# Performance work log

Hardware: AMD Instinct MI355X
Metric: run time of the kernel (lower is better)

Reference implementation:

```python
import jax, jax.numpy as jnp
import numpy as np

EPS = 1e-8


def l2norm(x, axis):
    # matches torch: x / (sqrt(sum(x^2)) + eps)
    return x / (jnp.sqrt(jnp.sum(x * x, axis=axis, keepdims=True)) + EPS)


def setup_inputs() -> dict:
    key = jax.random.key(0)
    k1, k2, k3, k4, k5 = jax.random.split(key, 5)
    I, C, L, R, D = 16, 32, 32, 36, 1024  # n_image, n_caption, max_words, n_regions, embed_dim
    img_emb = l2norm(jax.random.normal(k1, (I, R, D), jnp.float32), -1)
    cap_emb = l2norm(jax.random.normal(k2, (C, L, D), jnp.float32), -1)
    W_emb = jax.random.normal(k3, (D, D), jnp.float32)  # nn.Embedding weight, N(0,1) default init
    sim_map_w = 2.5 + 0.1 * jax.random.normal(k4, (1, D), jnp.float32)  # init_weight: normal(2.5, 0.1)
    temp_scale_w = jnp.full((1, 1), np.log(1.0 / 0.07), jnp.float32)    # init_weight
    temp_learnable_w = jnp.full((1, 1), 4.0, jnp.float32)               # init_weight
    cap_lens = jax.random.randint(k5, (C,), 4, L + 1, jnp.int32)        # ragged caption lengths in [4, L]
    return dict(img_emb=img_emb, cap_emb=cap_emb, W_emb=W_emb, sim_map_w=sim_map_w,
                temp_scale_w=temp_scale_w, temp_learnable_w=temp_learnable_w, cap_lens=cap_lens)


def reference(img_emb, cap_emb, W_emb, sim_map_w, temp_scale_w, temp_learnable_w, cap_lens):
    D = W_emb.shape[0]
    L = cap_emb.shape[1]
    # --- dimension-weight branch (caption-independent) ---
    # linspace(0, D, D).long(): last index is D (out of range in torch); gather with clip.
    idx = jnp.floor(jnp.linspace(0.0, D, D)).astype(jnp.int32)
    weights = jax.nn.sigmoid(jnp.take(W_emb, idx, axis=0, mode='clip'))  # (D, D)
    mean_p = jnp.mean(weights, axis=1)                  # (D,)
    std_p = jnp.std(weights, axis=1, ddof=1)            # torch.std is unbiased
    thres = mean_p + sim_map_w[0] * std_p               # (D,)
    values = jnp.exp(temp_learnable_w[0, 0]) * (weights - thres[:, None])
    mask_p = jnp.tanh(jnp.exp(values))
    Dlw = l2norm(mask_p * weights, axis=1)              # Dim_learned_weights (D, D)
    diag = Dlw.sum(0)                                   # Diagonal (D,); diag_embed matmul == elementwise scale
    smooth = jnp.exp(temp_scale_w[0, 0])
    # --- vectorized ragged per-caption cross attention ---
    wmask = (jnp.arange(L)[None, :] < cap_lens[:, None]).astype(cap_emb.dtype)  # (C, L)
    # attn[c,i,l,r] = tanh(sum_d cap[c,l,d] * diag[d] * img[i,r,d])
    attn = jnp.tanh(jnp.einsum('cld,ird->cilr', cap_emb, img_emb * diag))
    attn = jnp.where(attn >= 0, attn, 0.1 * attn) * wmask[:, None, :, None]  # LeakyReLU(0.1), zero padded words
    attn = attn / (jnp.sqrt(jnp.sum(attn * attn, axis=2, keepdims=True)) + EPS)  # l2norm over word dim
    attn = jax.nn.softmax(attn * smooth, axis=3)        # softmax over regions
    ctx = l2norm(jnp.einsum('cilr,ird->cild', attn, img_emb), axis=-1)  # Context_img
    sim_loc = ctx * cap_emb[:, None, :, :]
    sim_sub = jnp.einsum('cild,ed->cile', sim_loc, Dlw)  # sim_loc @ Dlw.T
    sim_vec = l2norm(sim_sub, axis=-1).sum(-1)           # (C, I, L)
    # mean over the n_word valid words of each caption
    sim = jnp.sum(sim_vec * wmask[:, None, :], axis=2) / cap_lens[:, None].astype(cap_emb.dtype)  # (C, I)
    return sim.T  # (n_image, n_caption), matching torch.cat(sim_all, 1)
```

## Files before the change

kernel.cpp:

```cpp
#include <hip/hip_runtime.h>
#include <hip/hip_bf16.h>

#define I_N 16
#define C_N 32
#define L_N 32
#define R_N 36
#define D_N 1024
#define EPSF 1e-8f

typedef _Float16 f16;
typedef __attribute__((ext_vector_type(8))) _Float16 half8;
typedef __attribute__((ext_vector_type(4))) float floatx4;

__device__ __forceinline__ void gl16(const f16* g, f16* l) {
  __builtin_amdgcn_global_load_lds(
      (const __attribute__((address_space(1))) void*)g,
      (__attribute__((address_space(3))) void*)l, 16, 0, 0);
}

__device__ __forceinline__ float fast_tanh(float x) {
  float q = __expf(-2.f * fabsf(x));
  float t = (1.f - q) / (1.f + q);
  return (x >= 0.f) ? t : -t;
}

__device__ __forceinline__ float blk_sum_256(float v, float* red) {
  #pragma unroll
  for (int off = 32; off > 0; off >>= 1) v += __shfl_down(v, off, 64);
  int wid = threadIdx.x >> 6;
  if ((threadIdx.x & 63) == 0) red[wid] = v;
  __syncthreads();
  float s = red[0] + red[1] + red[2] + red[3];
  __syncthreads();
  return s;
}

__global__ __launch_bounds__(256) void k_dlw(const float* __restrict__ W,
    const float* __restrict__ simw, const float* __restrict__ tlw,
    float* __restrict__ Dlw, f16* __restrict__ DlwH) {
  int row = blockIdx.x, tid = threadIdx.x;
  __shared__ float red[4];
  const float* Wr = W + (size_t)row * D_N;
  float w[4]; float p = 0.f;
  #pragma unroll
  for (int k = 0; k < 4; ++k) {
    int j = tid + k * 256;
    float x = Wr[j];
    w[k] = 1.f / (1.f + __expf(-x));
    p += w[k];
  }
  float S = blk_sum_256(p, red);
  float mean = S * (1.f / 1024.f);
  p = 0.f;
  #pragma unroll
  for (int k = 0; k < 4; ++k) { float d = w[k] - mean; p += d * d; }
  float S2 = blk_sum_256(p, red);
  float stdv = sqrtf(S2 * (1.f / 1023.f));
  float thres = mean + simw[row] * stdv;
  float eT = __expf(tlw[0]);
  float mw[4]; p = 0.f;
  #pragma unroll
  for (int k = 0; k < 4; ++k) {
    float val = eT * (w[k] - thres);
    float y = __expf(val);
    float q = __expf(-2.f * y);
    float mp = (1.f - q) / (1.f + q);
    mw[k] = mp * w[k];
    p += mw[k] * mw[k];
  }
  float S3 = blk_sum_256(p, red);
  float inv = 1.f / (sqrtf(S3) + EPSF);
  #pragma unroll
  for (int k = 0; k < 4; ++k) {
    int j = tid + k * 256;
    float v = mw[k] * inv;
    Dlw[(size_t)row * D_N + j] = v;
    DlwH[(size_t)row * D_N + j] = (f16)v;
  }
}

__global__ __launch_bounds__(256) void k_diag_part(const float* __restrict__ Dlw,
                                                   float* __restrict__ dpart) {
  int col = blockIdx.x * 256 + threadIdx.x;
  int p = blockIdx.y;
  float s = 0.f;
  #pragma unroll 8
  for (int r = p * 64; r < p * 64 + 64; ++r) s += Dlw[(size_t)r * D_N + col];
  dpart[(size_t)p * D_N + col] = s;
}

__global__ __launch_bounds__(256) void k_diag2p(const float* __restrict__ dpart,
    const int* __restrict__ lens, float* __restrict__ diag,
    int* __restrict__ pfx, int* __restrict__ mp) {
  if (blockIdx.x < 4) {
    int col = blockIdx.x * 256 + threadIdx.x;
    float s = 0.f;
    #pragma unroll
    for (int p = 0; p < 16; ++p) s += dpart[(size_t)p * D_N + col];
    diag[col] = s;
  } else if (threadIdx.x < 64) {
    int l = threadIdx.x;
    int v = (l < 32) ? lens[l] : 0;
    int s = v;
    #pragma unroll
    for (int off = 1; off < 32; off <<= 1) {
      int t = __shfl_up(s, off, 64);
      if (l >= off) s += t;
    }
    if (l < 32) pfx[l] = s - v;
    if (l == 31) { pfx[32] = s; mp[0] = s * 16; }
  }
}

__global__ __launch_bounds__(256) void k_prep(const float* __restrict__ cap,
    const float* __restrict__ img, const float* __restrict__ diag,
    f16* __restrict__ capH, f16* __restrict__ imgH, f16* __restrict__ imgdH) {
  int bid = blockIdx.x;
  if (bid < 1024) {
    size_t base = (size_t)bid * D_N;
    #pragma unroll
    for (int k = 0; k < 4; ++k) {
      int j = threadIdx.x + k * 256;
      capH[base + j] = (f16)cap[base + j];
    }
  } else if (bid < 1600) {
    size_t base = (size_t)(bid - 1024) * D_N;
    #pragma unroll
    for (int k = 0; k < 4; ++k) {
      int j = threadIdx.x + k * 256;
      imgH[base + j] = (f16)img[base + j];
    }
  } else {
    int row = bid - 1600;
    int i = row / 48, r = row % 48;
    size_t dst = (size_t)row * D_N;
    if (r < R_N) {
      size_t src = ((size_t)i * R_N + r) * D_N;
      #pragma unroll
      for (int k = 0; k < 4; ++k) {
        int j = threadIdx.x + k * 256;
        imgdH[dst + j] = (f16)(img[src + j] * diag[j]);
      }
    } else {
      #pragma unroll
      for (int k = 0; k < 4; ++k) {
        int j = threadIdx.x + k * 256;
        imgdH[dst + j] = (f16)0.f;
      }
    }
  }
}

__global__ __launch_bounds__(256) void k_qk(const f16* __restrict__ A,
    const f16* __restrict__ B, const int* __restrict__ lens,
    const float* __restrict__ tsw, float* __restrict__ pw) {
  int mt = blockIdx.x;
  int i  = blockIdx.y;
  int tid = threadIdx.x;
  int w = tid >> 6, lane = tid & 63;
  int l15 = lane & 15, h = lane >> 4;
  __shared__ __align__(16) f16 Als[64 * 32];
  __shared__ __align__(16) f16 Bls[48 * 32];
  __shared__ float att[64][49];
  __shared__ float cn[2][R_N];
  floatx4 acc[3];
  #pragma unroll
  for (int nf = 0; nf < 3; ++nf) acc[nf] = (floatx4)0.f;
  int arow = tid >> 2;
  int u = tid & 3;
  int vf = (u | ((arow & 1) << 2)) ^ ((arow >> 1) & 7);
  int wofs = (((arow & 62) | (vf >> 2)) * 32) + (vf & 3) * 8;
  const f16* Ag = A + (size_t)(mt * 64 + arow) * D_N + u * 8;
  const f16* Bg = B + (size_t)(i * 48 + arow) * D_N + u * 8;
  int v2 = (h | ((l15 & 1) << 2)) ^ ((l15 >> 1) & 7);
  int rbit = (v2 >> 2) & 1;
  int pun = (v2 & 3) * 8;
  int aoff = (w * 16 + (l15 & 14) + rbit) * 32 + pun;
  int boff[3];
  #pragma unroll
  for (int nf = 0; nf < 3; ++nf) boff[nf] = (nf * 16 + (l15 & 14) + rbit) * 32 + pun;
  for (int kk = 0; kk < D_N; kk += 32) {
    *(float4*)(&Als[wofs]) = *(const float4*)(Ag + kk);
    if (tid < 192) *(float4*)(&Bls[wofs]) = *(const float4*)(Bg + kk);
    __syncthreads();
    half8 a = *(const half8*)(&Als[aoff]);
    #pragma unroll
    for (int nf = 0; nf < 3; ++nf) {
      half8 b = *(const half8*)(&Bls[boff[nf]]);
      acc[nf] = __builtin_amdgcn_mfma_f32_16x16x32_f16(a, b, acc[nf], 0, 0, 0);
    }
    __syncthreads();
  }
  int len0 = lens[mt * 2], len1 = lens[mt * 2 + 1];
  #pragma unroll
  for (int nf = 0; nf < 3; ++nf)
    #pragma unroll
    for (int j = 0; j < 4; ++j) {
      int ml = w * 16 + h * 4 + j;
      int n = nf * 16 + l15;
      float t = fast_tanh(acc[nf][j]);
      float v = (t >= 0.f) ? t : 0.1f * t;
      int len = (ml >= 32) ? len1 : len0;
      if ((ml & 31) >= len || n >= R_N) v = 0.f;
      att[ml][n] = v;
    }
  __syncthreads();
  for (int e = tid; e < 2 * R_N; e += 256) {
    int cc = e / R_N, r = e % R_N;
    float s = 0.f;
    #pragma unroll
    for (int l = 0; l < 32; ++l) { float a = att[cc * 32 + l][r]; s += a * a; }
    cn[cc][r] = sqrtf(s) + EPSF;
  }
  __syncthreads();
  if (tid < 64) {
    int cc = tid >> 5, l = tid & 31;
    float smooth = __expf(tsw[0]);
    float mx = -3.4e38f;
    #pragma unroll
    for (int r = 0; r < R_N; ++r) {
      float z = att[tid][r] / cn[cc][r] * smooth;
      att[tid][r] = z;
      mx = fmaxf(mx, z);
    }
    float se = 0.f;
    #pragma unroll
    for (int r = 0; r < R_N; ++r) {
      float e2 = __expf(att[tid][r] - mx);
      att[tid][r] = e2;
      se += e2;
    }
    float inv = 1.f / se;
    float* dst = pw + ((size_t)i * 1024 + (mt * 2 + cc) * 32 + l) * R_N;
    #pragma unroll
    for (int r = 0; r < R_N; ++r) dst[r] = att[tid][r] * inv;
  }
}

__global__ __launch_bounds__(256) void k_ctx(const float* __restrict__ pw,
    const f16* __restrict__ imgH, const float* __restrict__ cap,
    const int* __restrict__ lens, const int* __restrict__ pfx,
    f16* __restrict__ slc) {
  int c  = blockIdx.x;
  int i  = blockIdx.y;
  int tid = threadIdx.x;
  int w = tid >> 6;
  int cg = tid & 63;
  int len = lens[c];
  int pf = pfx[c];
  __shared__ float pA[32][R_N];
  __shared__ __align__(16) f16 rows[R_N][1024];
  for (int e = tid; e < 32 * R_N; e += 256) {
    int rr = e / R_N, r = e % R_N;
    pA[rr][r] = pw[((size_t)i * 1024 + c * 32 + rr) * R_N + r];
  }
  const f16* base = imgH + (size_t)i * R_N * D_N;
  #pragma unroll
  for (int t = 0; t < 9; ++t) {
    int rr = w * 9 + t;
    const f16* src = base + (size_t)rr * D_N + cg * 8;
    gl16(src,       &rows[rr][0]);
    gl16(src + 512, &rows[rr][512]);
  }
  __syncthreads();
  int d0 = cg * 8, d1 = 512 + cg * 8;
  #pragma unroll
  for (int sub = 0; sub < 2; ++sub) {
    float acc[4][16];
    #pragma unroll
    for (int j = 0; j < 4; ++j)
      #pragma unroll
      for (int q = 0; q < 16; ++q) acc[j][q] = 0.f;
    for (int k = 0; k < R_N; ++k) {
      half8 h0 = *(const half8*)(&rows[k][d0]);
      half8 h1 = *(const half8*)(&rows[k][d1]);
      float bv[16];
      #pragma unroll
      for (int q = 0; q < 8; ++q) { bv[q] = (float)h0[q]; bv[8 + q] = (float)h1[q]; }
      #pragma unroll
      for (int j = 0; j < 4; ++j) {
        float a = pA[sub * 16 + w * 4 + j][k];
        #pragma unroll
        for (int q = 0; q < 16; ++q) acc[j][q] += a * bv[q];
      }
    }
    #pragma unroll
    for (int j = 0; j < 4; ++j) {
      int l = sub * 16 + w * 4 + j;
      float ss = 0.f;
      #pragma unroll
      for (int q = 0; q < 16; ++q) ss += acc[j][q] * acc[j][q];
      #pragma unroll
      for (int off = 1; off < 64; off <<= 1) ss += __shfl_xor(ss, off, 64);
      if (l < len) {
        float inv = 1.f / (sqrtf(ss) + EPSF);
        const float* capr = cap + ((size_t)c * L_N + l) * D_N;
        float4 c0 = *(const float4*)(capr + d0);
        float4 c1 = *(const float4*)(capr + d0 + 4);
        float4 c2 = *(const float4*)(capr + d1);
        float4 c3 = *(const float4*)(capr + d1 + 4);
        float cv[16] = {c0.x,c0.y,c0.z,c0.w, c1.x,c1.y,c1.z,c1.w,
                        c2.x,c2.y,c2.z,c2.w, c3.x,c3.y,c3.z,c3.w};
        union { f16 h[16]; float4 f4[2]; } u;
        #pragma unroll
        for (int q = 0; q < 16; ++q) u.h[q] = (f16)(acc[j][q] * inv * cv[q]);
        f16* dst = slc + ((size_t)((pf + l) * 16 + i)) * D_N;
        *(float4*)(dst + d0) = u.f4[0];
        *(float4*)(dst + d1) = u.f4[1];
      }
    }
  }
}

__global__ __launch_bounds__(256) void k_gemm(const f16* __restrict__ A,
    const f16* __restrict__ B, const int* __restrict__ mp,
    float* __restrict__ rs16, float* __restrict__ rq16) {
  int bx = blockIdx.x, by = blockIdx.y;
  int Mp = mp[0];
  int m0 = bx * 128, n0 = by * 128;
  if (m0 >= Mp) return;
  int tid = threadIdx.x;
  int w = tid >> 6, lane = tid & 63;
  int l15 = lane & 15, h = lane >> 4;
  int wm = w >> 1, wn = w & 1;
  __shared__ __align__(16) f16 AB[3][2][128 * 32];
  floatx4 acc[4][4];
  #pragma unroll
  for (int mf = 0; mf < 4; ++mf)
    #pragma unroll
    for (int nf = 0; nf < 4; ++nf) acc[mf][nf] = (floatx4)0.f;

  int r_p = lane >> 2, u_p = lane & 3;
  int sw = (r_p >> 1) & 7;
  int val = (u_p | ((r_p & 1) << 2)) ^ sw;
  int r_l = (r_p & 14) | (val >> 2);
  int u_l = val & 3;
  const f16* As0 = A + (size_t)(m0 + w * 32 +  0 + r_l) * D_N + u_l * 8;
  const f16* As1 = A + (size_t)(m0 + w * 32 + 16 + r_l) * D_N + u_l * 8;
  const f16* Bs0 = B + (size_t)(n0 + w * 32 +  0 + r_l) * D_N + u_l * 8;
  const f16* Bs1 = B + (size_t)(n0 + w * 32 + 16 + r_l) * D_N + u_l * 8;

  int v2 = (h | ((l15 & 1) << 2)) ^ ((l15 >> 1) & 7);
  int rbit = (v2 >> 2) & 1;
  int pun = (v2 & 3) * 8;
  int aoff[4], boff[4];
  #pragma unroll
  for (int f = 0; f < 4; ++f) {
    aoff[f] = (wm * 64 + f * 16 + (l15 & 14) + rbit) * 32 + pun;
    boff[f] = (wn * 64 + f * 16 + (l15 & 14) + rbit) * 32 + pun;
  }

  #define STAGE(kt, b) { \
    int kof = (kt) * 32; \
    gl16(As0 + kof, &AB[b][0][(w * 32 +  0) * 32]); \
    gl16(As1 + kof, &AB[b][0][(w * 32 + 16) * 32]); \
    gl16(Bs0 + kof, &AB[b][1][(w * 32 +  0) * 32]); \
    gl16(Bs1 + kof, &AB[b][1][(w * 32 + 16) * 32]); }

  #define COMPUTE(b) { \
    half8 af[4], bf[4]; \
    _Pragma("unroll") for (int f = 0; f < 4; ++f) af[f] = *(const half8*)(&AB[b][0][aoff[f]]); \
    _Pragma("unroll") for (int f = 0; f < 4; ++f) bf[f] = *(const half8*)(&AB[b][1][boff[f]]); \
    _Pragma("unroll") for (int mf = 0; mf < 4; ++mf) \
      _Pragma("unroll") for (int nf = 0; nf < 4; ++nf) \
        acc[mf][nf] = __builtin_amdgcn_mfma_f32_16x16x32_f16(af[mf], bf[nf], acc[mf][nf], 0, 0, 0); }

  STAGE(0, 0);
  STAGE(1, 1);
  int cur = 0, n2 = 2;
  for (int kk = 0; kk < 30; ++kk) {
    STAGE(kk + 2, n2);
    asm volatile("s_waitcnt vmcnt(8)" ::: "memory");
    __builtin_amdgcn_s_barrier();
    __builtin_amdgcn_sched_barrier(0);
    COMPUTE(cur);
    __builtin_amdgcn_s_barrier();
    cur = (cur == 2) ? 0 : cur + 1;
    n2  = (n2  == 2) ? 0 : n2  + 1;
  }
  asm volatile("s_waitcnt vmcnt(4)" ::: "memory");
  __builtin_amdgcn_s_barrier();
  __builtin_amdgcn_sched_barrier(0);
  COMPUTE(cur);
  __builtin_amdgcn_s_barrier();
  cur = (cur == 2) ? 0 : cur + 1;
  asm volatile("s_waitcnt vmcnt(0)" ::: "memory");
  __builtin_amdgcn_s_barrier();
  __builtin_amdgcn_sched_barrier(0);
  COMPUTE(cur);
  #undef STAGE
  #undef COMPUTE

  int slot = by * 2 + wn;
  #pragma unroll
  for (int mf = 0; mf < 4; ++mf)
    #pragma unroll
    for (int j = 0; j < 4; ++j) {
      float s = 0.f, q = 0.f;
      #pragma unroll
      for (int nf = 0; nf < 4; ++nf) { float v = acc[mf][nf][j]; s += v; q += v * v; }
      #pragma unroll
      for (int off = 1; off < 16; off <<= 1) { s += __shfl_xor(s, off, 64); q += __shfl_xor(q, off, 64); }
      if (l15 == 0) {
        int m = m0 + wm * 64 + mf * 16 + h * 4 + j;
        rs16[(size_t)slot * 16384 + m] = s;
        rq16[(size_t)slot * 16384 + m] = q;
      }
    }
}

__global__ __launch_bounds__(64) void k_final(const float* __restrict__ rs16,
    const float* __restrict__ rq16, const int* __restrict__ lens,
    const int* __restrict__ pfx, float* __restrict__ out) {
  int b = blockIdx.x;
  int c = b & 31;
  int l = threadIdx.x;
  int len = lens[c];
  float sv = 0.f;
  if (l < len) {
    int i = b >> 5;
    int row = (pfx[c] + l) * 16 + i;
    float rs = 0.f, rq = 0.f;
    #pragma unroll
    for (int s = 0; s < 16; ++s) {
      rs += rs16[(size_t)s * 16384 + row];
      rq += rq16[(size_t)s * 16384 + row];
    }
    sv = rs / (sqrtf(rq) + EPSF);
  }
  #pragma unroll
  for (int off = 32; off > 0; off >>= 1) sv += __shfl_down(sv, off, 64);
  if (l == 0) out[b] = sv / (float)len;
}

extern "C" void kernel_launch(void* const* d_in, const int* in_sizes, int n_in,
                              void* d_out, int out_size, void* d_ws, size_t ws_size,
                              hipStream_t stream) {
  const float* img  = (const float*)d_in[0];
  const float* cap  = (const float*)d_in[1];
  const float* W    = (const float*)d_in[2];
  const float* simw = (const float*)d_in[3];
  const float* tsw  = (const float*)d_in[4];
  const float* tlw  = (const float*)d_in[5];
  const int*   lens = (const int*)d_in[6];
  float* out = (float*)d_out;

  char* wsB = (char*)d_ws;
  if (ws_size < 51122176) return;
  float* Dlw   = (float*)(wsB + 0);
  f16*   DlwH  = (f16*)  (wsB + 4194304);
  float* diag  = (float*)(wsB + 6291456);
  f16*   capH  = (f16*)  (wsB + 6295552);
  f16*   imgdH = (f16*)  (wsB + 8392704);
  float* dpart = (float*)(wsB + 9965568);
  float* pw    = (float*)(wsB + 13111296);
  f16*   slc   = (f16*)  (wsB + 15470592);
  float* rs16  = (float*)(wsB + 49025024);
  float* rq16  = (float*)(wsB + 50073600);
  f16*   imgH  = (f16*)Dlw;
  int*   mp    = (int*)(wsB + 2097152);
  int*   pfx   = (int*)(wsB + 2097152 + 256);

  k_dlw<<<1024, 256, 0, stream>>>(W, simw, tlw, Dlw, DlwH);
  k_diag_part<<<dim3(4, 16), 256, 0, stream>>>(Dlw, dpart);
  k_diag2p<<<5, 256, 0, stream>>>(dpart, lens, diag, pfx, mp);
  k_prep<<<2368, 256, 0, stream>>>(cap, img, diag, capH, imgH, imgdH);
  k_qk<<<dim3(16, 16), 256, 0, stream>>>(capH, imgdH, lens, tsw, pw);
  k_ctx<<<dim3(32, 16), 256, 0, stream>>>(pw, imgH, cap, lens, pfx, slc);
  k_gemm<<<dim3(128, 8), 256, 0, stream>>>(slc, DlwH, mp, rs16, rq16);
  k_final<<<512, 64, 0, stream>>>(rs16, rq16, lens, pfx, out);
}
```

Baseline: 103.5 us.

## Apply diag scaling to captions and share padded fp16 image between kernels

The diagonal scale now multiplies the caption embeddings instead of the image embeddings. This removes the separate diag-scaled image copy, so one padded fp16 image buffer is built inside the Dlw kernel and used by both the attention and context kernels. The diag partial and final reductions are folded into a prefix kernel and a caption-scaling kernel, cutting the launch count from 8 to 7 and removing a full fp16 image conversion pass. Each caption-scaling block now redundantly sums 16 partial rows of diag, and the context kernel reads the image with a 48-row stride.

Measured after the change: 102.1 us. About the same (-1.4%).

```diff
diff --git a/kernel.cpp b/kernel.cpp
--- a/kernel.cpp
+++ b/kernel.cpp
@@ -37,8 +37,30 @@
 
 __global__ __launch_bounds__(256) void k_dlw(const float* __restrict__ W,
     const float* __restrict__ simw, const float* __restrict__ tlw,
-    float* __restrict__ Dlw, f16* __restrict__ DlwH) {
-  int row = blockIdx.x, tid = threadIdx.x;
+    const float* __restrict__ img,
+    float* __restrict__ Dlw, f16* __restrict__ DlwH, f16* __restrict__ imgP) {
+  int bid = blockIdx.x, tid = threadIdx.x;
+  if (bid >= 1024) {
+    int row = bid - 1024;
+    int i = row / 48, r = row % 48;
+    size_t dst = (size_t)row * D_N;
+    if (r < R_N) {
+      size_t src = ((size_t)i * R_N + r) * D_N;
+      #pragma unroll
+      for (int k = 0; k < 4; ++k) {
+        int j = tid + k * 256;
+        imgP[dst + j] = (f16)img[src + j];
+      }
+    } else {
+      #pragma unroll
+      for (int k = 0; k < 4; ++k) {
+        int j = tid + k * 256;
+        imgP[dst + j] = (f16)0.f;
+      }
+    }
+    return;
+  }
+  int row = bid;
   __shared__ float red[4];
   const float* Wr = W + (size_t)row * D_N;
   float w[4]; float p = 0.f;
@@ -79,25 +101,17 @@
   }
 }
 
-__global__ __launch_bounds__(256) void k_diag_part(const float* __restrict__ Dlw,
-                                                   float* __restrict__ dpart) {
-  int col = blockIdx.x * 256 + threadIdx.x;
-  int p = blockIdx.y;
-  float s = 0.f;
-  #pragma unroll 8
-  for (int r = p * 64; r < p * 64 + 64; ++r) s += Dlw[(size_t)r * D_N + col];
-  dpart[(size_t)p * D_N + col] = s;
-}
-
-__global__ __launch_bounds__(256) void k_diag2p(const float* __restrict__ dpart,
-    const int* __restrict__ lens, float* __restrict__ diag,
+__global__ __launch_bounds__(256) void k_dpp(const float* __restrict__ Dlw,
+    const int* __restrict__ lens, float* __restrict__ dpart,
     int* __restrict__ pfx, int* __restrict__ mp) {
-  if (blockIdx.x < 4) {
-    int col = blockIdx.x * 256 + threadIdx.x;
+  int bid = blockIdx.x;
+  if (bid < 64) {
+    int p = bid >> 2;
+    int col = (bid & 3) * 256 + threadIdx.x;
     float s = 0.f;
-    #pragma unroll
-    for (int p = 0; p < 16; ++p) s += dpart[(size_t)p * D_N + col];
-    diag[col] = s;
+    #pragma unroll 8
+    for (int r = p * 64; r < p * 64 + 64; ++r) s += Dlw[(size_t)r * D_N + col];
+    dpart[(size_t)p * D_N + col] = s;
   } else if (threadIdx.x < 64) {
     int l = threadIdx.x;
     int v = (l < 32) ? lens[l] : 0;
@@ -112,42 +126,24 @@
   }
 }
 
-__global__ __launch_bounds__(256) void k_prep(const float* __restrict__ cap,
-    const float* __restrict__ img, const float* __restrict__ diag,
-    f16* __restrict__ capH, f16* __restrict__ imgH, f16* __restrict__ imgdH) {
-  int bid = blockIdx.x;
-  if (bid < 1024) {
-    size_t base = (size_t)bid * D_N;
-    #pragma unroll
-    for (int k = 0; k < 4; ++k) {
-      int j = threadIdx.x + k * 256;
-      capH[base + j] = (f16)cap[base + j];
-    }
-  } else if (bid < 1600) {
-    size_t base = (size_t)(bid - 1024) * D_N;
-    #pragma unroll
-    for (int k = 0; k < 4; ++k) {
-      int j = threadIdx.x + k * 256;
-      imgH[base + j] = (f16)img[base + j];
-    }
-  } else {
-    int row = bid - 1600;
-    int i = row / 48, r = row % 48;
-    size_t dst = (size_t)row * D_N;
-    if (r < R_N) {
-      size_t src = ((size_t)i * R_N + r) * D_N;
-      #pragma unroll
-      for (int k = 0; k < 4; ++k) {
-        int j = threadIdx.x + k * 256;
-        imgdH[dst + j] = (f16)(img[src + j] * diag[j]);
-      }
-    } else {
-      #pragma unroll
-      for (int k = 0; k < 4; ++k) {
-        int j = threadIdx.x + k * 256;
-        imgdH[dst + j] = (f16)0.f;
-      }
-    }
+__global__ __launch_bounds__(256) void k_capd(const float* __restrict__ dpart,
+    const float* __restrict__ cap, f16* __restrict__ capD) {
+  __shared__ float dg[D_N];
+  int tid = threadIdx.x;
+  #pragma unroll
+  for (int k = 0; k < 4; ++k) {
+    int col = tid + k * 256;
+    float s = 0.f;
+    #pragma unroll
+    for (int p = 0; p < 16; ++p) s += dpart[(size_t)p * D_N + col];
+    dg[col] = s;
+  }
+  __syncthreads();
+  size_t base = (size_t)blockIdx.x * D_N;
+  #pragma unroll
+  for (int k = 0; k < 4; ++k) {
+    int j = tid + k * 256;
+    capD[base + j] = (f16)(cap[base + j] * dg[j]);
   }
 }
 
@@ -238,7 +234,7 @@
 }
 
 __global__ __launch_bounds__(256) void k_ctx(const float* __restrict__ pw,
-    const f16* __restrict__ imgH, const float* __restrict__ cap,
+    const f16* __restrict__ imgP, const float* __restrict__ cap,
     const int* __restrict__ lens, const int* __restrict__ pfx,
     f16* __restrict__ slc) {
   int c  = blockIdx.x;
@@ -254,7 +250,7 @@
     int rr = e / R_N, r = e % R_N;
     pA[rr][r] = pw[((size_t)i * 1024 + c * 32 + rr) * R_N + r];
   }
-  const f16* base = imgH + (size_t)i * R_N * D_N;
+  const f16* base = imgP + (size_t)i * 48 * D_N;
   #pragma unroll
   for (int t = 0; t < 9; ++t) {
     int rr = w * 9 + t;
@@ -449,24 +445,21 @@
   if (ws_size < 51122176) return;
   float* Dlw   = (float*)(wsB + 0);
   f16*   DlwH  = (f16*)  (wsB + 4194304);
-  float* diag  = (float*)(wsB + 6291456);
-  f16*   capH  = (f16*)  (wsB + 6295552);
-  f16*   imgdH = (f16*)  (wsB + 8392704);
+  f16*   capD  = (f16*)  (wsB + 6295552);
+  f16*   imgP  = (f16*)  (wsB + 8392704);
   float* dpart = (float*)(wsB + 9965568);
+  int*   mp    = (int*)  (wsB + 10031104);
+  int*   pfx   = (int*)  (wsB + 10031360);
   float* pw    = (float*)(wsB + 13111296);
   f16*   slc   = (f16*)  (wsB + 15470592);
   float* rs16  = (float*)(wsB + 49025024);
   float* rq16  = (float*)(wsB + 50073600);
-  f16*   imgH  = (f16*)Dlw;
-  int*   mp    = (int*)(wsB + 2097152);
-  int*   pfx   = (int*)(wsB + 2097152 + 256);
-
-  k_dlw<<<1024, 256, 0, stream>>>(W, simw, tlw, Dlw, DlwH);
-  k_diag_part<<<dim3(4, 16), 256, 0, stream>>>(Dlw, dpart);
-  k_diag2p<<<5, 256, 0, stream>>>(dpart, lens, diag, pfx, mp);
-  k_prep<<<2368, 256, 0, stream>>>(cap, img, diag, capH, imgH, imgdH);
-  k_qk<<<dim3(16, 16), 256, 0, stream>>>(capH, imgdH, lens, tsw, pw);
-  k_ctx<<<dim3(32, 16), 256, 0, stream>>>(pw, imgH, cap, lens, pfx, slc);
+
+  k_dlw<<<1792, 256, 0, stream>>>(W, simw, tlw, img, Dlw, DlwH, imgP);
+  k_dpp<<<65, 256, 0, stream>>>(Dlw, lens, dpart, pfx, mp);
+  k_capd<<<1024, 256, 0, stream>>>(dpart, cap, capD);
+  k_qk<<<dim3(16, 16), 256, 0, stream>>>(capD, imgP, lens, tsw, pw);
+  k_ctx<<<dim3(32, 16), 256, 0, stream>>>(pw, imgP, cap, lens, pfx, slc);
   k_gemm<<<dim3(128, 8), 256, 0, stream>>>(slc, DlwH, mp, rs16, rq16);
   k_final<<<512, 64, 0, stream>>>(rs16, rq16, lens, pfx, out);
 }
```
